# Kernel tuning notes

Hardware: AMD Instinct MI355X
Metric: run time of the kernel (lower is better)

## Reference

```python
import jax, jax.numpy as jnp
import numpy as np
import math

DIM = 1536
HEAD_DIM = 128
N_HEADS = DIM // HEAD_DIM
B, S = 2, 2048
F, H, W = 8, 16, 16  # F*H*W == S
MAX_POS = 1024
EPS = 1e-6


def _make_freqs():
    # complex rotary freqs per Wan convention, split [22,21,21] over head_dim/2=64
    c = HEAD_DIM // 2
    sizes = [c - 2 * (c // 3), c // 3, c // 3]
    theta = 10000.0
    parts = []
    for s in sizes:
        inv = 1.0 / theta ** (np.arange(s, dtype=np.float64) / s)
        ang = np.arange(MAX_POS, dtype=np.float64)[:, None] * inv[None, :]
        parts.append(np.stack([np.cos(ang), np.sin(ang)], axis=-1))
    return jnp.asarray(np.concatenate(parts, axis=1), dtype=jnp.float32)  # [MAX_POS, 64, 2]


def setup_inputs() -> dict:
    key = jax.random.key(0)
    ks = jax.random.split(key, 12)
    std = 1.0 / math.sqrt(DIM)
    inp = {
        "x": jax.random.normal(ks[0], (B, S, DIM), jnp.float32),
        "seq_lens": jnp.full((B,), S, jnp.int32),
        "grid_sizes": jnp.tile(jnp.array([[F, H, W]], jnp.int32), (B, 1)),
        "freqs": _make_freqs(),
        "Wq": jax.random.normal(ks[1], (DIM, DIM), jnp.float32) * std,
        "bq": jnp.zeros((DIM,), jnp.float32),
        "Wk": jax.random.normal(ks[2], (DIM, DIM), jnp.float32) * std,
        "bk": jnp.zeros((DIM,), jnp.float32),
        "Wv": jax.random.normal(ks[3], (DIM, DIM), jnp.float32) * std,
        "bv": jnp.zeros((DIM,), jnp.float32),
        "Wo": jax.random.normal(ks[4], (DIM, DIM), jnp.float32) * std,
        "bo": jnp.zeros((DIM,), jnp.float32),
        "wq_norm": jnp.ones((DIM,), jnp.float32),
        "wk_norm": jnp.ones((DIM,), jnp.float32),
    }
    return inp


def _rmsnorm(x, w):
    x32 = x.astype(jnp.float32)
    return x32 * jax.lax.rsqrt(jnp.mean(x32 * x32, axis=-1, keepdims=True) + EPS) * w


def _rope_apply(x, grid_sizes, freqs):
    # x: [B, S, N, D]; grid sizes uniform across batch -> vectorized (no per-sample loop)
    f, h, w = (int(v) for v in np.asarray(grid_sizes)[0])
    s_rot = f * h * w
    Bx, Sx, N, D = x.shape
    c = D // 2
    s0, s1 = c - 2 * (c // 3), c // 3
    cos, sin = freqs[..., 0], freqs[..., 1]

    def grid_cs(t):  # build [s_rot, c] table
        tf = jnp.broadcast_to(t[:f, None, None, :s0], (f, h, w, s0))
        th = jnp.broadcast_to(t[None, :h, None, s0:s0 + s1], (f, h, w, s1))
        tw = jnp.broadcast_to(t[None, None, :w, s0 + s1:s0 + 2 * s1], (f, h, w, s1))
        return jnp.concatenate([tf, th, tw], axis=-1).reshape(s_rot, 1, c)

    fc, fs = grid_cs(cos), grid_cs(sin)  # [s_rot, 1, c]
    xr = x[:, :s_rot].astype(jnp.float32).reshape(Bx, s_rot, N, c, 2)
    a, b = xr[..., 0], xr[..., 1]
    out = jnp.stack([a * fc - b * fs, a * fs + b * fc], axis=-1).reshape(Bx, s_rot, N, D)
    if s_rot < Sx:
        out = jnp.concatenate([out, x[:, s_rot:].astype(jnp.float32)], axis=1)
    return out


def reference(x, seq_lens, grid_sizes, freqs, Wq, bq, Wk, bk, Wv, bv, Wo, bo, wq_norm, wk_norm):
    Bx, Sx, dim = x.shape
    N, D = N_HEADS, HEAD_DIM
    q = _rmsnorm(x @ Wq.T + bq, wq_norm).reshape(Bx, Sx, N, D)
    k = _rmsnorm(x @ Wk.T + bk, wk_norm).reshape(Bx, Sx, N, D)
    v = (x @ Wv.T + bv).reshape(Bx, Sx, N, D)
    q = _rope_apply(q, grid_sizes, freqs)
    k = _rope_apply(k, grid_sizes, freqs)
    scores = jnp.einsum("bsnd,btnd->bnst", q, k) / math.sqrt(D)  # [B,N,S,S]
    kmask = jnp.arange(Sx)[None, :] < seq_lens[:, None]          # [B,S] over keys
    scores = jnp.where(kmask[:, None, None, :], scores, -1e30)
    attn = jax.nn.softmax(scores, axis=-1)
    out = jnp.einsum("bnst,btnd->bsnd", attn, v).reshape(Bx, Sx, dim)
    return out @ Wo.T + bo
```

## Files before the change

### kernel.cpp

```cpp
#include <hip/hip_runtime.h>

typedef __attribute__((ext_vector_type(8))) short bf16x8;
typedef __attribute__((ext_vector_type(8))) unsigned short ushort8;
typedef __attribute__((ext_vector_type(4))) float f32x4;
typedef __attribute__((ext_vector_type(16))) float f32x16;
typedef unsigned short u16;
typedef unsigned int u32;

__device__ inline float bf2f(u16 u) {
    unsigned int x = ((unsigned int)u) << 16;
    float f; __builtin_memcpy(&f, &x, 4); return f;
}
__device__ inline u16 f2bf(float f) {
    unsigned int x; __builtin_memcpy(&x, &f, 4);
    unsigned int r = (x + 0x7FFFu + ((x >> 16) & 1u)) >> 16;
    return (u16)r;
}
__device__ inline u32 cvtpk(float lo, float hi) {
    u32 r;
    asm("v_cvt_pk_bf16_f32 %0, %1, %2" : "=v"(r) : "v"(lo), "v"(hi));
    return r;
}
__device__ inline void store_out(u16* p, float v) { *p = f2bf(v); }
__device__ inline void store_out(float* p, float v) { *p = v; }

__global__ __launch_bounds__(256) void f32_to_bf16_kernel(const float* __restrict__ src,
                                                          u16* __restrict__ dst, int n8) {
    int i = blockIdx.x * 256 + threadIdx.x;
    if (i >= n8) return;
    float4 a = *(const float4*)(src + (size_t)i * 8);
    float4 b = *(const float4*)(src + (size_t)i * 8 + 4);
    ushort8 o;
    o[0] = f2bf(a.x); o[1] = f2bf(a.y); o[2] = f2bf(a.z); o[3] = f2bf(a.w);
    o[4] = f2bf(b.x); o[5] = f2bf(b.y); o[6] = f2bf(b.z); o[7] = f2bf(b.w);
    *(ushort8*)(dst + (size_t)i * 8) = o;
}

__global__ __launch_bounds__(256) void wconv_kernel(const float* __restrict__ Wq, const float* __restrict__ Wk,
                                                    const float* __restrict__ Wv, const float* __restrict__ Wo,
                                                    u16* __restrict__ wqkv, u16* __restrict__ wob) {
    int i = blockIdx.x * 256 + threadIdx.x;
    int seg = i / 294912, j = i - seg * 294912;
    const float* src = (seg == 0) ? Wq : (seg == 1) ? Wk : (seg == 2) ? Wv : Wo;
    u16* dst = (seg < 3) ? (wqkv + (size_t)seg * 2359296) : wob;
    float4 a = *(const float4*)(src + (size_t)j * 8);
    float4 b = *(const float4*)(src + (size_t)j * 8 + 4);
    ushort8 o;
    o[0] = f2bf(a.x); o[1] = f2bf(a.y); o[2] = f2bf(a.z); o[3] = f2bf(a.w);
    o[4] = f2bf(b.x); o[5] = f2bf(b.y); o[6] = f2bf(b.z); o[7] = f2bf(b.w);
    *(ushort8*)(dst + (size_t)j * 8) = o;
}

__global__ __launch_bounds__(256) void build_rope_kernel(const float* __restrict__ freqs,
                                                         float* __restrict__ rope) {
    int i = blockIdx.x * 256 + threadIdx.x;
    int s = i >> 6, j = i & 63;
    int fi = s >> 8, hi = (s >> 4) & 15, wi = s & 15;
    int pos = (j < 22) ? fi : ((j < 43) ? hi : wi);
    rope[s * 128 + j * 2]     = freqs[pos * 128 + j * 2];
    rope[s * 128 + j * 2 + 1] = freqs[pos * 128 + j * 2 + 1];
}

template <typename OutT>
__global__ __launch_bounds__(512) void gemm256(const u16* __restrict__ A, const u16* __restrict__ Bw,
                                               const float* __restrict__ bias, OutT* __restrict__ C,
                                               int M, int N, int K, int nby) {
    __shared__ __align__(16) char smem[131072];
    const int tid = threadIdx.x;
    const int wid = tid >> 6, l = tid & 63;
    const int wr = wid >> 2, wc = wid & 3;
    const int lg = l >> 4, li = l & 15;
    const int nwg = gridDim.x;
    const int cpx = nwg >> 3;
    int swz = (blockIdx.x & 7) * cpx + (blockIdx.x >> 3);
    const int row0 = (swz / nby) * 256, col0 = (swz % nby) * 256;
    const int NT = K >> 6;

    f32x4 acc[8][4] = {};

    auto STAGE_HT = [&](int mat, int t, int kk) {
        const u16* src = mat ? Bw : A;
        const int r0 = mat ? col0 : row0;
        const int base = (mat ? 65536 : 0) + (t & 1) * 32768 + kk * 16384;
#pragma unroll
        for (int j = 0; j < 2; ++j) {
            int bi = j * 512 + tid;
            int r = bi >> 2;
            int clog = (bi & 3) ^ (r & 3);
            __builtin_amdgcn_global_load_lds(
                (const __attribute__((address_space(1))) void*)(src + (size_t)(r0 + r) * K + t * 64 + kk * 32 + clog * 8),
                (__attribute__((address_space(3))) void*)(smem + base + j * 8192 + wid * 1024), 16, 0, 0);
        }
    };
    auto LDA = [&](bf16x8* af, int t, int kk, int mh) {
        const u16* R = (const u16*)(smem + (t & 1) * 32768 + kk * 16384);
#pragma unroll
        for (int mm = 0; mm < 4; ++mm) {
            int row = wr * 128 + (mh * 4 + mm) * 16 + li;
            af[mm] = *(const bf16x8*)(R + row * 32 + ((lg ^ (li & 3)) * 8));
        }
    };
    auto LDB = [&](bf16x8* bf, int t, int kk) {
        const u16* R = (const u16*)(smem + 65536 + (t & 1) * 32768 + kk * 16384);
#pragma unroll
        for (int nn = 0; nn < 4; ++nn) {
            int row = wc * 64 + nn * 16 + li;
            bf[nn] = *(const bf16x8*)(R + row * 32 + ((lg ^ (li & 3)) * 8));
        }
    };

    STAGE_HT(0, 0, 0); STAGE_HT(1, 0, 0); STAGE_HT(0, 0, 1); STAGE_HT(1, 0, 1);
    STAGE_HT(0, 1, 0); STAGE_HT(1, 1, 0);
    asm volatile("s_waitcnt vmcnt(4)" ::: "memory");
    __builtin_amdgcn_s_barrier();
    __builtin_amdgcn_sched_barrier(0);

    bf16x8 af[4], bf[4];
    for (int t = 0; t < NT; ++t) {
        LDA(af, t, 0, 0); LDB(bf, t, 0);
        if (t + 1 < NT) STAGE_HT(0, t + 1, 1);
        __builtin_amdgcn_s_barrier();
        asm volatile("s_waitcnt lgkmcnt(0)" ::: "memory");
        __builtin_amdgcn_sched_barrier(0);
        __builtin_amdgcn_s_setprio(1);
#pragma unroll
        for (int mm = 0; mm < 4; ++mm)
#pragma unroll
            for (int nn = 0; nn < 4; ++nn)
                acc[mm][nn] = __builtin_amdgcn_mfma_f32_16x16x32_bf16(af[mm], bf[nn], acc[mm][nn], 0, 0, 0);
        __builtin_amdgcn_s_setprio(0);
        __builtin_amdgcn_sched_barrier(0);
        __builtin_amdgcn_s_barrier();
        LDA(af, t, 0, 1);
        if (t + 1 < NT) STAGE_HT(1, t + 1, 1);
        __builtin_amdgcn_s_barrier();
        asm volatile("s_waitcnt lgkmcnt(0)" ::: "memory");
        __builtin_amdgcn_sched_barrier(0);
        __builtin_amdgcn_s_setprio(1);
#pragma unroll
        for (int mm = 0; mm < 4; ++mm)
#pragma unroll
            for (int nn = 0; nn < 4; ++nn)
                acc[4 + mm][nn] = __builtin_amdgcn_mfma_f32_16x16x32_bf16(af[mm], bf[nn], acc[4 + mm][nn], 0, 0, 0);
        __builtin_amdgcn_s_setprio(0);
        __builtin_amdgcn_sched_barrier(0);
        __builtin_amdgcn_s_barrier();
        LDA(af, t, 1, 0); LDB(bf, t, 1);
        if (t + 2 < NT) STAGE_HT(0, t + 2, 0);
        __builtin_amdgcn_s_barrier();
        asm volatile("s_waitcnt lgkmcnt(0)" ::: "memory");
        __builtin_amdgcn_sched_barrier(0);
        __builtin_amdgcn_s_setprio(1);
#pragma unroll
        for (int mm = 0; mm < 4; ++mm)
#pragma unroll
            for (int nn = 0; nn < 4; ++nn)
                acc[mm][nn] = __builtin_amdgcn_mfma_f32_16x16x32_bf16(af[mm], bf[nn], acc[mm][nn], 0, 0, 0);
        __builtin_amdgcn_s_setprio(0);
        __builtin_amdgcn_sched_barrier(0);
        __builtin_amdgcn_s_barrier();
        LDA(af, t, 1, 1);
        if (t + 2 < NT) STAGE_HT(1, t + 2, 0);
        __builtin_amdgcn_s_barrier();
        asm volatile("s_waitcnt lgkmcnt(0)" ::: "memory");
        __builtin_amdgcn_sched_barrier(0);
        __builtin_amdgcn_s_setprio(1);
#pragma unroll
        for (int mm = 0; mm < 4; ++mm)
#pragma unroll
            for (int nn = 0; nn < 4; ++nn)
                acc[4 + mm][nn] = __builtin_amdgcn_mfma_f32_16x16x32_bf16(af[mm], bf[nn], acc[4 + mm][nn], 0, 0, 0);
        __builtin_amdgcn_s_setprio(0);
        __builtin_amdgcn_sched_barrier(0);
        if (t + 2 < NT) { asm volatile("s_waitcnt vmcnt(4)" ::: "memory"); }
        else            { asm volatile("s_waitcnt vmcnt(0)" ::: "memory"); }
        __builtin_amdgcn_s_barrier();
        __builtin_amdgcn_sched_barrier(0);
    }

#pragma unroll
    for (int m = 0; m < 8; ++m) {
#pragma unroll
        for (int n = 0; n < 4; ++n) {
#pragma unroll
            for (int j = 0; j < 4; ++j) {
                int r = row0 + wr * 128 + m * 16 + lg * 4 + j;
                int cc = col0 + wc * 64 + n * 16 + li;
                float v = acc[m][n][j] + bias[cc];
                store_out(&C[(size_t)r * N + cc], v);
            }
        }
    }
}

template <typename OutT>
__global__ __launch_bounds__(256) void gemm_bt(const u16* __restrict__ A, const u16* __restrict__ Bw,
                                               const float* __restrict__ bias, OutT* __restrict__ C,
                                               int M, int N, int K) {
    __shared__ __align__(16) u16 As[3][4096];
    __shared__ __align__(16) u16 Bs[3][4096];
    const int tid = threadIdx.x;
    const int w = tid >> 6, l = tid & 63;
    const int lg = l >> 4, li = l & 15;
    const int row0 = blockIdx.x * 128, col0 = blockIdx.y * 128;
    const int wr = (w >> 1) * 64, wc = (w & 1) * 64;
    const int nt = K >> 5;

    f32x4 acc[4][4] = {};

    auto STAGE = [&](int bi, int t) {
        int k0 = t << 5;
#pragma unroll
        for (int c = 0; c < 2; ++c) {
            int idx = c * 256 + tid;
            int r = idx >> 2;
            int clog = (idx & 3) ^ (r & 3);
            __builtin_amdgcn_global_load_lds(
                (const __attribute__((address_space(1))) void*)(A + (size_t)(row0 + r) * K + k0 + clog * 8),
                (__attribute__((address_space(3))) void*)((char*)&As[0][0] + bi * 8192 + c * 4096 + w * 1024), 16, 0, 0);
            __builtin_amdgcn_global_load_lds(
                (const __attribute__((address_space(1))) void*)(Bw + (size_t)(col0 + r) * K + k0 + clog * 8),
                (__attribute__((address_space(3))) void*)((char*)&Bs[0][0] + bi * 8192 + c * 4096 + w * 1024), 16, 0, 0);
        }
    };

    STAGE(0, 0);
    STAGE(1, 1);
    for (int tb = 0; tb < nt; tb += 3) {
#pragma unroll
        for (int j = 0; j < 3; ++j) {
            const int t = tb + j;
            if (t + 2 < nt) {
                STAGE((j + 2) % 3, t + 2);
                asm volatile("s_waitcnt vmcnt(8)" ::: "memory");
            } else if (t + 1 < nt) {
                asm volatile("s_waitcnt vmcnt(4)" ::: "memory");
            } else {
                asm volatile("s_waitcnt vmcnt(0)" ::: "memory");
            }
            __builtin_amdgcn_s_barrier();
            __builtin_amdgcn_sched_barrier(0);
            const u16* as = &As[j][0];
            const u16* bs = &Bs[j][0];
            bf16x8 af[4], bfr[4];
#pragma unroll
            for (int m = 0; m < 4; ++m) af[m] = *(const bf16x8*)(as + (wr + m * 16 + li) * 32 + ((lg ^ (li & 3)) * 8));
#pragma unroll
            for (int n = 0; n < 4; ++n) bfr[n] = *(const bf16x8*)(bs + (wc + n * 16 + li) * 32 + ((lg ^ (li & 3)) * 8));
#pragma unroll
            for (int m = 0; m < 4; ++m)
#pragma unroll
                for (int n = 0; n < 4; ++n)
                    acc[m][n] = __builtin_amdgcn_mfma_f32_16x16x32_bf16(af[m], bfr[n], acc[m][n], 0, 0, 0);
            __builtin_amdgcn_sched_barrier(0);
            __builtin_amdgcn_s_barrier();
        }
    }

#pragma unroll
    for (int m = 0; m < 4; ++m) {
#pragma unroll
        for (int n = 0; n < 4; ++n) {
#pragma unroll
            for (int j = 0; j < 4; ++j) {
                int r = row0 + wr + m * 16 + lg * 4 + j;
                int cc = col0 + wc + n * 16 + li;
                float v = acc[m][n][j] + bias[cc];
                store_out(&C[(size_t)r * N + cc], v);
            }
        }
    }
}

__global__ __launch_bounds__(256) void rmsrope_kernel(const u16* __restrict__ qkv,
                                                      const float* __restrict__ wq_n,
                                                      const float* __restrict__ wk_n,
                                                      const float* __restrict__ rope,
                                                      u16* __restrict__ qh, u16* __restrict__ kh) {
    int row = blockIdx.x;
    int b = row >> 11, s = row & 2047;
    int t = threadIdx.x;
    const u16* pr = qkv + (size_t)row * 4608;
    int c0 = t * 6;

    float q[6], k[6];
#pragma unroll
    for (int i = 0; i < 3; ++i) {
        ushort2 uq = *(const ushort2*)(pr + c0 + 2 * i);
        ushort2 uk = *(const ushort2*)(pr + 1536 + c0 + 2 * i);
        q[2 * i] = bf2f(uq.x); q[2 * i + 1] = bf2f(uq.y);
        k[2 * i] = bf2f(uk.x); k[2 * i + 1] = bf2f(uk.y);
    }
    float sq = 0.f, sk = 0.f;
#pragma unroll
    for (int i = 0; i < 6; ++i) { sq += q[i] * q[i]; sk += k[i] * k[i]; }
#pragma unroll
    for (int off = 32; off >= 1; off >>= 1) {
        sq += __shfl_down(sq, off);
        sk += __shfl_down(sk, off);
    }
    __shared__ float red[8];
    int w = t >> 6, l = t & 63;
    if (l == 0) { red[w] = sq; red[w + 4] = sk; }
    __syncthreads();
    float rq = rsqrtf((red[0] + red[1] + red[2] + red[3]) * (1.0f / 1536.0f) + 1e-6f);
    float rk = rsqrtf((red[4] + red[5] + red[6] + red[7]) * (1.0f / 1536.0f) + 1e-6f);

#pragma unroll
    for (int i = 0; i < 3; ++i) {
        int c = c0 + 2 * i;
        int h = c >> 7, d = c & 127;
        float cs = rope[s * 128 + d];
        float sn = rope[s * 128 + d + 1];
        float qa = q[2 * i] * rq * wq_n[c], qb = q[2 * i + 1] * rq * wq_n[c + 1];
        float ka = k[2 * i] * rk * wk_n[c], kb = k[2 * i + 1] * rk * wk_n[c + 1];
        size_t o = ((size_t)(b * 12 + h) * 2048 + s) * 128 + d;
        ushort2 qo, ko;
        qo.x = f2bf(qa * cs - qb * sn); qo.y = f2bf(qa * sn + qb * cs);
        ko.x = f2bf(ka * cs - kb * sn); ko.y = f2bf(ka * sn + kb * cs);
        *(ushort2*)(qh + o) = qo;
        *(ushort2*)(kh + o) = ko;
    }
}

__global__ __launch_bounds__(256) void vtrans_kernel(const u16* __restrict__ qkv,
                                                     u16* __restrict__ vt) {
    const int s0 = blockIdx.x * 64;
    const int d0 = blockIdx.y * 64;
    const int bh = blockIdx.z;
    const int b = bh / 12, h = bh % 12;
    const int t = threadIdx.x;

    __shared__ __align__(16) u16 L[64 * 72];

#pragma unroll
    for (int j = 0; j < 2; ++j) {
        int idx = j * 256 + t;
        int s = idx >> 3, c8 = idx & 7;
        ushort8 v8 = *(const ushort8*)(qkv + (size_t)(b * 2048 + s0 + s) * 4608 + 3072 + h * 128 + d0 + c8 * 8);
        int pb = c8 ^ ((s >> 3) & 7);
        *(ushort8*)(L + s * 72 + pb * 8) = v8;
    }
    __syncthreads();
#pragma unroll
    for (int j = 0; j < 2; ++j) {
        int idx = j * 256 + t;
        int d = idx >> 3, s8 = idx & 7;
        ushort8 o;
#pragma unroll
        for (int i = 0; i < 8; ++i) {
            int ps = s8 * 8 + i;
            int v4 = ps & 15;
            int ls = (ps & ~15) | (v4 & 3) | ((v4 & 4) << 1) | ((v4 & 8) >> 1);
            o[i] = L[ls * 72 + ((((d >> 3) ^ (ls >> 3)) & 7) << 3) + (d & 7)];
        }
        *(ushort8*)(vt + (size_t)bh * 128 * 2048 + (size_t)(d0 + d) * 2048 + s0 + s8 * 8) = o;
    }
}

__global__ __launch_bounds__(256, 2) void attn_kernel(const u16* __restrict__ qh, const u16* __restrict__ kh,
                                                      const u16* __restrict__ vt, const int* __restrict__ seq_lens,
                                                      u16* __restrict__ aout) {
    const int qt = blockIdx.x;
    const int bh = blockIdx.y;
    const int b = bh / 12, h = bh % 12;
    const int tid = threadIdx.x;
    const int w = tid >> 6, l = tid & 63;
    const int q5 = l & 31;
    const int hi = l >> 5;
    const int seqlen = seq_lens[b];

    __shared__ __align__(16) char smem[65536];

    const size_t hbase = (size_t)bh * 2048 * 128;
    const u16* kb = kh + hbase;
    const u16* vtb = vt + hbase;

    const int qrow = qt * 128 + w * 32 + q5;
    bf16x8 qf[8];
    {
        const u16* qp = qh + hbase + (size_t)qrow * 128 + hi * 8;
#pragma unroll
        for (int kd = 0; kd < 8; ++kd) qf[kd] = *(const bf16x8*)(qp + kd * 16);
    }

    auto STAGE = [&](int bi, int kv0) {
#pragma unroll
        for (int i = 0; i < 4; ++i) {
            int p = i * 256 + tid;
            int kr = p >> 4, kc = p & 15;
            __builtin_amdgcn_global_load_lds(
                (const __attribute__((address_space(1))) void*)(kb + (size_t)(kv0 + kr) * 128 + ((kc ^ (kr & 15)) << 3)),
                (__attribute__((address_space(3))) void*)(smem + bi * 16384 + i * 4096 + w * 1024), 16, 0, 0);
            int vr = p >> 3, vc = p & 7;
            __builtin_amdgcn_global_load_lds(
                (const __attribute__((address_space(1))) void*)(vtb + (size_t)vr * 2048 + kv0 + ((vc ^ (vr & 7)) << 3)),
                (__attribute__((address_space(3))) void*)(smem + 32768 + bi * 16384 + i * 4096 + w * 1024), 16, 0, 0);
        }
    };

    f32x16 oacc[4] = {};
    float m_run = -3e38f, l_run = 0.f;
    const float c2 = 0.08838834764831845f * 1.44269504088896341f;

    STAGE(0, 0);
    for (int t = 0; t < 32; ++t) {
        const int cur = t & 1;
        const int kv0 = t * 64;
        if (t < 31) {
            STAGE(cur ^ 1, kv0 + 64);
            asm volatile("s_waitcnt vmcnt(8)" ::: "memory");
        } else {
            asm volatile("s_waitcnt vmcnt(0)" ::: "memory");
        }
        __builtin_amdgcn_s_barrier();
        __builtin_amdgcn_sched_barrier(0);

        const u16* Ks = (const u16*)(smem + cur * 16384);
        const u16* Vs = (const u16*)(smem + 32768 + cur * 16384);

        f32x16 sacc[2] = {};
        __builtin_amdgcn_s_setprio(1);
#pragma unroll
        for (int tt = 0; tt < 2; ++tt) {
            int row = tt * 32 + q5;
#pragma unroll
            for (int kd = 0; kd < 8; ++kd) {
                int bk = (2 * kd + hi) ^ (q5 & 15);
                bf16x8 kf = *(const bf16x8*)(Ks + row * 128 + bk * 8);
                sacc[tt] = __builtin_amdgcn_mfma_f32_32x32x16_bf16(kf, qf[kd], sacc[tt], 0, 0, 0);
            }
        }
        __builtin_amdgcn_s_setprio(0);

        if (kv0 + 64 > seqlen) {
#pragma unroll
            for (int tt = 0; tt < 2; ++tt)
#pragma unroll
                for (int m = 0; m < 4; ++m)
#pragma unroll
                    for (int r = 0; r < 4; ++r) {
                        int kv = kv0 + tt * 32 + m * 8 + hi * 4 + r;
                        if (kv >= seqlen) sacc[tt][m * 4 + r] = -1e30f;
                    }
        }

        float pmax = sacc[0][0];
#pragma unroll
        for (int tt = 0; tt < 2; ++tt)
#pragma unroll
            for (int r = 0; r < 16; ++r) pmax = fmaxf(pmax, sacc[tt][r]);
        pmax = fmaxf(pmax, __shfl_xor(pmax, 32));

        int defer = __all(pmax <= m_run + 62.7f);
        if (!defer) {
            float mnew = fmaxf(m_run, pmax);
            float alpha = __builtin_amdgcn_exp2f((m_run - mnew) * c2);
#pragma unroll
            for (int dt = 0; dt < 4; ++dt)
#pragma unroll
                for (int r = 0; r < 16; ++r) oacc[dt][r] *= alpha;
            l_run *= alpha;
            m_run = mnew;
        }

        float ls = 0.f;
        u32 Wp[2][4][2];
#pragma unroll
        for (int tt = 0; tt < 2; ++tt)
#pragma unroll
            for (int m = 0; m < 4; ++m) {
                float p0 = __builtin_amdgcn_exp2f((sacc[tt][4 * m + 0] - m_run) * c2);
                float p1 = __builtin_amdgcn_exp2f((sacc[tt][4 * m + 1] - m_run) * c2);
                float p2 = __builtin_amdgcn_exp2f((sacc[tt][4 * m + 2] - m_run) * c2);
                float p3 = __builtin_amdgcn_exp2f((sacc[tt][4 * m + 3] - m_run) * c2);
                ls += (p0 + p1) + (p2 + p3);
                Wp[tt][m][0] = cvtpk(p0, p1);
                Wp[tt][m][1] = cvtpk(p2, p3);
            }
        ls += __shfl_xor(ls, 32);
        l_run += ls;

        __builtin_amdgcn_s_setprio(1);
#pragma unroll
        for (int tt = 0; tt < 2; ++tt)
#pragma unroll
            for (int c = 0; c < 2; ++c) {
                union { u32 u[4]; bf16x8 v; } pu;
                pu.u[0] = Wp[tt][2 * c][0]; pu.u[1] = Wp[tt][2 * c][1];
                pu.u[2] = Wp[tt][2 * c + 1][0]; pu.u[3] = Wp[tt][2 * c + 1][1];
                int bk = 4 * tt + 2 * c + hi;
#pragma unroll
                for (int dt = 0; dt < 4; ++dt) {
                    int drow = dt * 32 + q5;
                    int pb = bk ^ (drow & 7);
                    bf16x8 vf = *(const bf16x8*)(Vs + drow * 64 + pb * 8);
                    oacc[dt] = __builtin_amdgcn_mfma_f32_32x32x16_bf16(vf, pu.v, oacc[dt], 0, 0, 0);
                }
            }
        __builtin_amdgcn_s_setprio(0);
        __builtin_amdgcn_sched_barrier(0);
        __builtin_amdgcn_s_barrier();
    }

    __syncthreads();
    u32* Lq = (u32*)smem + w * 2144;
    float inv_l = 1.0f / l_run;
#pragma unroll
    for (int dt = 0; dt < 4; ++dt)
#pragma unroll
        for (int m = 0; m < 4; ++m) {
            u32 w0 = cvtpk(oacc[dt][4 * m + 0] * inv_l, oacc[dt][4 * m + 1] * inv_l);
            u32 w1 = cvtpk(oacc[dt][4 * m + 2] * inv_l, oacc[dt][4 * m + 3] * inv_l);
            int widx = dt * 16 + 4 * m + 2 * hi;
            Lq[q5 * 67 + widx] = w0;
            Lq[q5 * 67 + widx + 1] = w1;
        }
    __builtin_amdgcn_s_waitcnt(0);
#pragma unroll
    for (int pp = 0; pp < 8; ++pp) {
        int qq = pp * 4 + (l >> 4);
        int cc = l & 15;
        union { u32 u[4]; ushort8 v; } ou;
        ou.u[0] = Lq[qq * 67 + cc * 4 + 0];
        ou.u[1] = Lq[qq * 67 + cc * 4 + 1];
        ou.u[2] = Lq[qq * 67 + cc * 4 + 2];
        ou.u[3] = Lq[qq * 67 + cc * 4 + 3];
        size_t off = ((size_t)(b * 2048 + qt * 128 + w * 32 + qq)) * 1536 + h * 128 + cc * 8;
        *(ushort8*)(aout + off) = ou.v;
    }
}

extern "C" void kernel_launch(void* const* d_in, const int* in_sizes, int n_in,
                              void* d_out, int out_size, void* d_ws, size_t ws_size,
                              hipStream_t stream) {
    const float* x    = (const float*)d_in[0];
    const int* seqlen = (const int*)d_in[1];
    const float* freqs = (const float*)d_in[3];
    const float* Wq = (const float*)d_in[4];  const float* bq = (const float*)d_in[5];
    const float* Wk = (const float*)d_in[6];  const float* bk = (const float*)d_in[7];
    const float* Wv = (const float*)d_in[8];  const float* bv = (const float*)d_in[9];
    const float* Wo = (const float*)d_in[10]; const float* bo = (const float*)d_in[11];
    const float* wqn = (const float*)d_in[12];
    const float* wkn = (const float*)d_in[13];
    float* out = (float*)d_out;

    char* ws = (char*)d_ws;
    u16*   xb   = (u16*)(ws);
    u16*   wqkv = (u16*)(ws + 12582912);
    u16*   wob  = (u16*)(ws + 26738688);
    float* bqkv = (float*)(ws + 31457280);
    float* rope = (float*)(ws + 31475712);
    u16*   qkv  = (u16*)(ws + 32524288);
    u16*   qhb  = (u16*)(ws + 70273024);
    u16*   khb  = (u16*)(ws + 82855936);
    u16*   vtb  = (u16*)(ws + 95438848);
    u16*   aob  = (u16*)(ws + 108021760);

    f32_to_bf16_kernel<<<3072, 256, 0, stream>>>(x, xb, 786432);
    wconv_kernel<<<4608, 256, 0, stream>>>(Wq, Wk, Wv, Wo, wqkv, wob);
    hipMemcpyAsync(bqkv,        bq, 1536 * 4, hipMemcpyDeviceToDevice, stream);
    hipMemcpyAsync(bqkv + 1536, bk, 1536 * 4, hipMemcpyDeviceToDevice, stream);
    hipMemcpyAsync(bqkv + 3072, bv, 1536 * 4, hipMemcpyDeviceToDevice, stream);
    build_rope_kernel<<<512, 256, 0, stream>>>(freqs, rope);

    gemm256<u16><<<288, 512, 0, stream>>>(xb, wqkv, bqkv, qkv, 4096, 4608, 1536, 18);
    rmsrope_kernel<<<4096, 256, 0, stream>>>(qkv, wqn, wkn, rope, qhb, khb);
    vtrans_kernel<<<dim3(32, 2, 24), 256, 0, stream>>>(qkv, vtb);
    attn_kernel<<<dim3(16, 24), 256, 0, stream>>>(qhb, khb, vtb, seqlen, aob);
    gemm_bt<float><<<dim3(32, 12), 256, 0, stream>>>(aob, wob, bo, out, 4096, 1536, 1536);
}
```

Baseline: 246.7 us.

## Halve gemm256 K-tile to 32 with 64KB LDS and new swizzle

Cuts the 256x256 GEMM's k-step from 64 to 32 and shrinks shared memory from 128KB to 64KB. The double buffer now holds one 32-wide k-slice per stage, and the kernel waits for all outstanding loads (vmcnt(0)) at the end of each iteration. The aim is to allow more resident workgroups per CU. The LDS XOR swizzle changes from row&3 to (row>>1)&3 in both GEMM kernels to reduce bank conflicts. In exchange there are twice as many iterations and barriers, and prefetch depth drops, so less global-load latency is hidden.

```diff
diff --git a/kernel.cpp b/kernel.cpp
--- a/kernel.cpp
+++ b/kernel.cpp
@@ -65,7 +65,7 @@
 __global__ __launch_bounds__(512) void gemm256(const u16* __restrict__ A, const u16* __restrict__ Bw,
                                                const float* __restrict__ bias, OutT* __restrict__ C,
                                                int M, int N, int K, int nby) {
-    __shared__ __align__(16) char smem[131072];
+    __shared__ __align__(16) char smem[65536];
     const int tid = threadIdx.x;
     const int wid = tid >> 6, l = tid & 63;
     const int wr = wid >> 2, wc = wid & 3;
@@ -74,51 +74,51 @@
     const int cpx = nwg >> 3;
     int swz = (blockIdx.x & 7) * cpx + (blockIdx.x >> 3);
     const int row0 = (swz / nby) * 256, col0 = (swz % nby) * 256;
-    const int NT = K >> 6;
+    const int NT = K >> 5;
 
     f32x4 acc[8][4] = {};
 
-    auto STAGE_HT = [&](int mat, int t, int kk) {
+    auto STAGE = [&](int mat, int t) {
         const u16* src = mat ? Bw : A;
         const int r0 = mat ? col0 : row0;
-        const int base = (mat ? 65536 : 0) + (t & 1) * 32768 + kk * 16384;
+        const int base = (mat ? 32768 : 0) + (t & 1) * 16384;
 #pragma unroll
         for (int j = 0; j < 2; ++j) {
             int bi = j * 512 + tid;
             int r = bi >> 2;
-            int clog = (bi & 3) ^ (r & 3);
+            int clog = (bi & 3) ^ ((r >> 1) & 3);
             __builtin_amdgcn_global_load_lds(
-                (const __attribute__((address_space(1))) void*)(src + (size_t)(r0 + r) * K + t * 64 + kk * 32 + clog * 8),
+                (const __attribute__((address_space(1))) void*)(src + (size_t)(r0 + r) * K + t * 32 + clog * 8),
                 (__attribute__((address_space(3))) void*)(smem + base + j * 8192 + wid * 1024), 16, 0, 0);
         }
     };
-    auto LDA = [&](bf16x8* af, int t, int kk, int mh) {
-        const u16* R = (const u16*)(smem + (t & 1) * 32768 + kk * 16384);
+    const int rchunk = (lg ^ ((li >> 1) & 3)) * 8;
+    auto LDA = [&](bf16x8* af, int t, int mh) {
+        const u16* R = (const u16*)(smem + (t & 1) * 16384);
 #pragma unroll
         for (int mm = 0; mm < 4; ++mm) {
             int row = wr * 128 + (mh * 4 + mm) * 16 + li;
-            af[mm] = *(const bf16x8*)(R + row * 32 + ((lg ^ (li & 3)) * 8));
+            af[mm] = *(const bf16x8*)(R + row * 32 + rchunk);
         }
     };
-    auto LDB = [&](bf16x8* bf, int t, int kk) {
-        const u16* R = (const u16*)(smem + 65536 + (t & 1) * 32768 + kk * 16384);
+    auto LDB = [&](bf16x8* bf, int t) {
+        const u16* R = (const u16*)(smem + 32768 + (t & 1) * 16384);
 #pragma unroll
         for (int nn = 0; nn < 4; ++nn) {
             int row = wc * 64 + nn * 16 + li;
-            bf[nn] = *(const bf16x8*)(R + row * 32 + ((lg ^ (li & 3)) * 8));
+            bf[nn] = *(const bf16x8*)(R + row * 32 + rchunk);
         }
     };
 
-    STAGE_HT(0, 0, 0); STAGE_HT(1, 0, 0); STAGE_HT(0, 0, 1); STAGE_HT(1, 0, 1);
-    STAGE_HT(0, 1, 0); STAGE_HT(1, 1, 0);
-    asm volatile("s_waitcnt vmcnt(4)" ::: "memory");
+    STAGE(0, 0); STAGE(1, 0);
+    asm volatile("s_waitcnt vmcnt(0)" ::: "memory");
     __builtin_amdgcn_s_barrier();
     __builtin_amdgcn_sched_barrier(0);
 
     bf16x8 af[4], bf[4];
     for (int t = 0; t < NT; ++t) {
-        LDA(af, t, 0, 0); LDB(bf, t, 0);
-        if (t + 1 < NT) STAGE_HT(0, t + 1, 1);
+        LDA(af, t, 0); LDB(bf, t);
+        if (t + 1 < NT) STAGE(0, t + 1);
         __builtin_amdgcn_s_barrier();
         asm volatile("s_waitcnt lgkmcnt(0)" ::: "memory");
         __builtin_amdgcn_sched_barrier(0);
@@ -131,8 +131,8 @@
         __builtin_amdgcn_s_setprio(0);
         __builtin_amdgcn_sched_barrier(0);
         __builtin_amdgcn_s_barrier();
-        LDA(af, t, 0, 1);
-        if (t + 1 < NT) STAGE_HT(1, t + 1, 1);
+        LDA(af, t, 1);
+        if (t + 1 < NT) STAGE(1, t + 1);
         __builtin_amdgcn_s_barrier();
         asm volatile("s_waitcnt lgkmcnt(0)" ::: "memory");
         __builtin_amdgcn_sched_barrier(0);
@@ -144,36 +144,7 @@
                 acc[4 + mm][nn] = __builtin_amdgcn_mfma_f32_16x16x32_bf16(af[mm], bf[nn], acc[4 + mm][nn], 0, 0, 0);
         __builtin_amdgcn_s_setprio(0);
         __builtin_amdgcn_sched_barrier(0);
-        __builtin_amdgcn_s_barrier();
-        LDA(af, t, 1, 0); LDB(bf, t, 1);
-        if (t + 2 < NT) STAGE_HT(0, t + 2, 0);
-        __builtin_amdgcn_s_barrier();
-        asm volatile("s_waitcnt lgkmcnt(0)" ::: "memory");
-        __builtin_amdgcn_sched_barrier(0);
-        __builtin_amdgcn_s_setprio(1);
-#pragma unroll
-        for (int mm = 0; mm < 4; ++mm)
-#pragma unroll
-            for (int nn = 0; nn < 4; ++nn)
-                acc[mm][nn] = __builtin_amdgcn_mfma_f32_16x16x32_bf16(af[mm], bf[nn], acc[mm][nn], 0, 0, 0);
-        __builtin_amdgcn_s_setprio(0);
-        __builtin_amdgcn_sched_barrier(0);
-        __builtin_amdgcn_s_barrier();
-        LDA(af, t, 1, 1);
-        if (t + 2 < NT) STAGE_HT(1, t + 2, 0);
-        __builtin_amdgcn_s_barrier();
-        asm volatile("s_waitcnt lgkmcnt(0)" ::: "memory");
-        __builtin_amdgcn_sched_barrier(0);
-        __builtin_amdgcn_s_setprio(1);
-#pragma unroll
-        for (int mm = 0; mm < 4; ++mm)
-#pragma unroll
-            for (int nn = 0; nn < 4; ++nn)
-                acc[4 + mm][nn] = __builtin_amdgcn_mfma_f32_16x16x32_bf16(af[mm], bf[nn], acc[4 + mm][nn], 0, 0, 0);
-        __builtin_amdgcn_s_setprio(0);
-        __builtin_amdgcn_sched_barrier(0);
-        if (t + 2 < NT) { asm volatile("s_waitcnt vmcnt(4)" ::: "memory"); }
-        else            { asm volatile("s_waitcnt vmcnt(0)" ::: "memory"); }
+        asm volatile("s_waitcnt vmcnt(0)" ::: "memory");
         __builtin_amdgcn_s_barrier();
         __builtin_amdgcn_sched_barrier(0);
     }
@@ -214,7 +185,7 @@
         for (int c = 0; c < 2; ++c) {
             int idx = c * 256 + tid;
             int r = idx >> 2;
-            int clog = (idx & 3) ^ (r & 3);
+            int clog = (idx & 3) ^ ((r >> 1) & 3);
             __builtin_amdgcn_global_load_lds(
                 (const __attribute__((address_space(1))) void*)(A + (size_t)(row0 + r) * K + k0 + clog * 8),
                 (__attribute__((address_space(3))) void*)((char*)&As[0][0] + bi * 8192 + c * 4096 + w * 1024), 16, 0, 0);
@@ -224,6 +195,7 @@
         }
     };
 
+    const int rchunk = (lg ^ ((li >> 1) & 3)) * 8;
     STAGE(0, 0);
     STAGE(1, 1);
     for (int tb = 0; tb < nt; tb += 3) {
@@ -244,9 +216,9 @@
             const u16* bs = &Bs[j][0];
             bf16x8 af[4], bfr[4];
 #pragma unroll
-            for (int m = 0; m < 4; ++m) af[m] = *(const bf16x8*)(as + (wr + m * 16 + li) * 32 + ((lg ^ (li & 3)) * 8));
-#pragma unroll
-            for (int n = 0; n < 4; ++n) bfr[n] = *(const bf16x8*)(bs + (wc + n * 16 + li) * 32 + ((lg ^ (li & 3)) * 8));
+            for (int m = 0; m < 4; ++m) af[m] = *(const bf16x8*)(as + (wr + m * 16 + li) * 32 + rchunk);
+#pragma unroll
+            for (int n = 0; n < 4; ++n) bfr[n] = *(const bf16x8*)(bs + (wc + n * 16 + li) * 32 + rchunk);
 #pragma unroll
             for (int m = 0; m < 4; ++m)
 #pragma unroll
```

Measured after the change: 249.7 us. About the same (+1.2%).
